# Kernel tuning notes

Hardware: AMD Instinct MI355X
Metric: run time of the kernel (lower is better)

## Reference

```python
import jax, jax.numpy as jnp
import numpy as np

MSG_DIM = 100
REG_WEIGHT = 1.0
N_NODES = 100000
N_EDGES = 1000000
D_FEAT = 6
HIDDEN = 300
OUT_DIM = 2


def setup_inputs() -> dict:
    key = jax.random.key(0)
    ks = jax.random.split(key, 10)
    def glorot(k, shape):
        fan_in = shape[0]
        return jax.random.normal(k, shape, dtype=jnp.float32) / jnp.sqrt(jnp.float32(fan_in))
    return {
        "x": jax.random.normal(ks[0], (N_NODES, D_FEAT), dtype=jnp.float32),
        "edge_index": jax.random.randint(ks[1], (2, N_EDGES), 0, N_NODES, dtype=jnp.int64)
            if jax.config.jax_enable_x64 else jax.random.randint(ks[1], (2, N_EDGES), 0, N_NODES, dtype=jnp.int32),
        "y": jax.random.normal(ks[2], (N_NODES, OUT_DIM), dtype=jnp.float32),
        "target": jax.random.normal(ks[3], (N_NODES, OUT_DIM), dtype=jnp.float32),
        "W1": glorot(ks[4], (2 * D_FEAT, HIDDEN)),
        "b1": jnp.zeros((HIDDEN,), dtype=jnp.float32),
        "W2": glorot(ks[5], (HIDDEN, HIDDEN)),
        "b2": jnp.zeros((HIDDEN,), dtype=jnp.float32),
        "W3": glorot(ks[6], (HIDDEN, 2 * MSG_DIM)),
        "b3": jnp.zeros((2 * MSG_DIM,), dtype=jnp.float32),
    }


def reference(x, edge_index, y, target, W1, b1, W2, b2, W3, b3):
    # MAE term: sum |y - target| / n_nodes
    base_loss = jnp.sum(jnp.abs(y - target)) / y.shape[0]
    # Gather sender/receiver node features per edge and concat -> [E, 2*d_feat]
    e = jnp.concatenate([x[edge_index[0]], x[edge_index[1]]], axis=1)
    # edge_model MLP: 2*d_feat -> 300 -> 300 -> 2*msg_dim
    h = jax.nn.relu(e @ W1 + b1)
    h = jax.nn.relu(h @ W2 + b2)
    messages = h @ W3 + b3  # [E, 2*msg_dim]
    mu = messages[:, :MSG_DIM]
    logvar = messages[:, MSG_DIM:]
    kl_reg = jnp.sum(0.5 * (mu * mu + jnp.exp(logvar) - logvar - 1.0)) / messages.shape[0]
    return base_loss + REG_WEIGHT * kl_reg
```

## Files before the change

kernel.cpp:

```cpp
#include <hip/hip_runtime.h>

#define N_NODES 100000
#define N_EDGES 1000000
#define D_FEAT  6
#define HIDDEN  300
#define HID_P   320
#define MSG     100
#define OUTC    200
#define OUTC_P  208
#define MT      64
#define NT_H    (HID_P/16)
#define NT_M    (OUTC_P/16)
#define KS_H    (HID_P/32)

typedef __bf16 bf16_t;
typedef __bf16 bf16x8 __attribute__((ext_vector_type(8)));
typedef __bf16 bf16x4 __attribute__((ext_vector_type(4)));
typedef float  floatx4 __attribute__((ext_vector_type(4)));

#define PREP_BLOCKS 700
#define LOSS_BLOCKS 200
__global__ void prep_kernel(const float* __restrict__ W1, const float* __restrict__ W2,
                            const float* __restrict__ W3, bf16_t* __restrict__ W1P,
                            bf16_t* __restrict__ W2P, bf16_t* __restrict__ W3P,
                            const float* __restrict__ y, const float* __restrict__ t,
                            float* __restrict__ out) {
    if (blockIdx.x >= PREP_BLOCKS) {
        float s = 0.f;
        for (int i = (blockIdx.x - PREP_BLOCKS) * blockDim.x + threadIdx.x;
             i < N_NODES * 2; i += LOSS_BLOCKS * blockDim.x)
            s += fabsf(y[i] - t[i]);
        #pragma unroll
        for (int off = 32; off; off >>= 1) s += __shfl_down(s, off);
        __shared__ float red[4];
        if ((threadIdx.x & 63) == 0) red[threadIdx.x >> 6] = s;
        __syncthreads();
        if (threadIdx.x == 0)
            atomicAdd(out, (red[0] + red[1] + red[2] + red[3]) * (1.0f / N_NODES));
        return;
    }
    const int n1 = NT_H * 512;
    const int n2 = NT_H * KS_H * 512;
    const int n3 = NT_M * KS_H * 512;
    const int total = n1 + n2 + n3;
    for (int id = blockIdx.x * blockDim.x + threadIdx.x; id < total;
         id += PREP_BLOCKS * blockDim.x) {
        if (id < n1) {
            int nt = id >> 9, rem = id & 511, lane = rem >> 3, j = rem & 7;
            int n = nt * 16 + (lane & 15), k = (lane >> 4) * 8 + j;
            float v = (n < HIDDEN && k < 2 * D_FEAT) ? W1[k * HIDDEN + n] : 0.f;
            W1P[id] = (bf16_t)v;
        } else if (id < n1 + n2) {
            int r = id - n1;
            int chunk = r >> 9, rem = r & 511, lane = rem >> 3, j = rem & 7;
            int ks = chunk % KS_H, nt = chunk / KS_H;
            int n = nt * 16 + (lane & 15), k = ks * 32 + (lane >> 4) * 8 + j;
            float v = (n < HIDDEN && k < HIDDEN) ? W2[k * HIDDEN + n] : 0.f;
            W2P[r] = (bf16_t)v;
        } else {
            int r = id - n1 - n2;
            int chunk = r >> 9, rem = r & 511, lane = rem >> 3, j = rem & 7;
            int ks = chunk % KS_H, nt = chunk / KS_H;
            int n = nt * 16 + (lane & 15), k = ks * 32 + (lane >> 4) * 8 + j;
            float v = (n < OUTC && k < HIDDEN) ? W3[k * OUTC + n] : 0.f;
            W3P[r] = (bf16_t)v;
        }
    }
}

__global__ __launch_bounds__(512, 6) void mlp_kernel(
    const float* __restrict__ x, const int* __restrict__ ei,
    const bf16_t* __restrict__ W1P, const bf16_t* __restrict__ W2P,
    const bf16_t* __restrict__ W3P,
    const float* __restrict__ b1, const float* __restrict__ b2,
    const float* __restrict__ b3, float* __restrict__ out) {
    __shared__ __align__(16) bf16_t A1f[4 * 64 * 8];
    __shared__ __align__(16) bf16_t Hf[4 * KS_H * 64 * 8];
    __shared__ float red[8];

    const int tid  = threadIdx.x;
    const int w    = tid >> 6, lane = tid & 63;
    const int q    = lane >> 4, l16 = lane & 15;
    const int cnt_h = (w < 4) ? 3 : 2;
    const int cnt_m = (w >= 3) ? 2 : 1;
    const long e0 = (long)blockIdx.x * MT;

    *(ulong*)&A1f[tid * 4] = 0ul;
    __syncthreads();
    if (tid < 2 * MT) {
        int m = tid >> 1, side = tid & 1;
        int node = ei[(long)side * N_EDGES + e0 + m];
        const float* xr = x + (long)node * D_FEAT;
        int et = m >> 4, ml = m & 15;
        #pragma unroll
        for (int c = 0; c < D_FEAT; c++) {
            int k = side * D_FEAT + c;
            int lp = ml + 16 * (k >> 3);
            A1f[(et * 64 + lp) * 8 + (k & 7)] = (bf16_t)xr[c];
        }
    }
    __syncthreads();

    floatx4 acc1[3][4];
    {
        bf16x8 hb[4];
        #pragma unroll
        for (int e = 0; e < 4; e++)
            hb[e] = *(const bf16x8*)&A1f[(e * 64 + lane) * 8];
        #pragma unroll
        for (int t = 0; t < 3; t++) {
            if (t < cnt_h) {
                bf16x8 wf = *(const bf16x8*)&W1P[((w + 8 * t) * 64 + lane) * 8];
                #pragma unroll
                for (int e = 0; e < 4; e++) {
                    floatx4 z = {0.f, 0.f, 0.f, 0.f};
                    acc1[t][e] = __builtin_amdgcn_mfma_f32_16x16x32_bf16(wf, hb[e], z, 0, 0, 0);
                }
            }
        }
    }
    #pragma unroll
    for (int t = 0; t < 3; t++) {
        if (t < cnt_h) {
            int n0 = (w + 8 * t) * 16 + 4 * q;
            floatx4 bv = (n0 < HIDDEN) ? *(const floatx4*)&b1[n0]
                                       : (floatx4){0.f, 0.f, 0.f, 0.f};
            int ks = n0 >> 5, lp = l16 + 16 * ((n0 >> 3) & 3), j0 = n0 & 7;
            #pragma unroll
            for (int e = 0; e < 4; e++) {
                bf16x4 pk;
                #pragma unroll
                for (int r = 0; r < 4; r++)
                    pk[r] = (bf16_t)fmaxf(acc1[t][e][r] + bv[r], 0.f);
                *(bf16x4*)&Hf[((e * KS_H + ks) * 64 + lp) * 8 + j0] = pk;
            }
        }
    }
    __syncthreads();

    floatx4 acc2[3][4];
    #pragma unroll
    for (int t = 0; t < 3; t++)
        #pragma unroll
        for (int e = 0; e < 4; e++) acc2[t][e] = (floatx4){0.f, 0.f, 0.f, 0.f};
    #pragma unroll 2
    for (int ks = 0; ks < KS_H; ks++) {
        bf16x8 hb[4];
        #pragma unroll
        for (int e = 0; e < 4; e++)
            hb[e] = *(const bf16x8*)&Hf[((e * KS_H + ks) * 64 + lane) * 8];
        #pragma unroll
        for (int t = 0; t < 3; t++) {
            if (t < cnt_h) {
                bf16x8 wf = *(const bf16x8*)&W2P[(((w + 8 * t) * KS_H + ks) * 64 + lane) * 8];
                #pragma unroll
                for (int e = 0; e < 4; e++)
                    acc2[t][e] = __builtin_amdgcn_mfma_f32_16x16x32_bf16(wf, hb[e], acc2[t][e], 0, 0, 0);
            }
        }
    }
    __syncthreads();
    #pragma unroll
    for (int t = 0; t < 3; t++) {
        if (t < cnt_h) {
            int n0 = (w + 8 * t) * 16 + 4 * q;
            floatx4 bv = (n0 < HIDDEN) ? *(const floatx4*)&b2[n0]
                                       : (floatx4){0.f, 0.f, 0.f, 0.f};
            int ks = n0 >> 5, lp = l16 + 16 * ((n0 >> 3) & 3), j0 = n0 & 7;
            #pragma unroll
            for (int e = 0; e < 4; e++) {
                bf16x4 pk;
                #pragma unroll
                for (int r = 0; r < 4; r++)
                    pk[r] = (bf16_t)fmaxf(acc2[t][e][r] + bv[r], 0.f);
                *(bf16x4*)&Hf[((e * KS_H + ks) * 64 + lp) * 8 + j0] = pk;
            }
        }
    }
    __syncthreads();

    floatx4 acc3[2][4];
    #pragma unroll
    for (int t = 0; t < 2; t++)
        #pragma unroll
        for (int e = 0; e < 4; e++) acc3[t][e] = (floatx4){0.f, 0.f, 0.f, 0.f};
    #pragma unroll 2
    for (int ks = 0; ks < KS_H; ks++) {
        bf16x8 hb[4];
        #pragma unroll
        for (int e = 0; e < 4; e++)
            hb[e] = *(const bf16x8*)&Hf[((e * KS_H + ks) * 64 + lane) * 8];
        #pragma unroll
        for (int t = 0; t < 2; t++) {
            if (t < cnt_m) {
                bf16x8 wf = *(const bf16x8*)&W3P[(((w + 5 * t) * KS_H + ks) * 64 + lane) * 8];
                #pragma unroll
                for (int e = 0; e < 4; e++)
                    acc3[t][e] = __builtin_amdgcn_mfma_f32_16x16x32_bf16(wf, hb[e], acc3[t][e], 0, 0, 0);
            }
        }
    }
    float s = 0.f;
    #pragma unroll
    for (int t = 0; t < 2; t++) {
        if (t < cnt_m) {
            int n0 = (w + 5 * t) * 16 + 4 * q;
            if (n0 < OUTC) {
                floatx4 bv = *(const floatx4*)&b3[n0];
                bool is_mu = (n0 < MSG);
                #pragma unroll
                for (int e = 0; e < 4; e++)
                    #pragma unroll
                    for (int r = 0; r < 4; r++) {
                        float v = acc3[t][e][r] + bv[r];
                        if (is_mu) s += 0.5f * v * v;
                        else       s += 0.5f * (__expf(v) - v - 1.f);
                    }
            }
        }
    }
    #pragma unroll
    for (int off = 32; off; off >>= 1) s += __shfl_down(s, off);
    if (lane == 0) red[w] = s;
    __syncthreads();
    if (tid == 0) {
        float t2 = 0.f;
        #pragma unroll
        for (int i = 0; i < 8; i++) t2 += red[i];
        atomicAdd(out, t2 * (1.0f / N_EDGES));
    }
}

extern "C" void kernel_launch(void* const* d_in, const int* in_sizes, int n_in,
                              void* d_out, int out_size, void* d_ws, size_t ws_size,
                              hipStream_t stream) {
    const float* x      = (const float*)d_in[0];
    const int*   ei     = (const int*)d_in[1];
    const float* y      = (const float*)d_in[2];
    const float* target = (const float*)d_in[3];
    const float* W1     = (const float*)d_in[4];
    const float* b1     = (const float*)d_in[5];
    const float* W2     = (const float*)d_in[6];
    const float* b2     = (const float*)d_in[7];
    const float* W3     = (const float*)d_in[8];
    const float* b3     = (const float*)d_in[9];
    float* out = (float*)d_out;

    bf16_t* W1P = (bf16_t*)d_ws;
    bf16_t* W2P = W1P + NT_H * 512;
    bf16_t* W3P = W2P + NT_H * KS_H * 512;

    hipMemsetAsync(d_out, 0, sizeof(float), stream);
    prep_kernel<<<PREP_BLOCKS + LOSS_BLOCKS, 256, 0, stream>>>(
        W1, W2, W3, W1P, W2P, W3P, y, target, out);
    mlp_kernel<<<N_EDGES / MT, 512, 0, stream>>>(x, ei, W1P, W2P, W3P, b1, b2, b3, out);
}
```

Before: 458.8 us.

## Halve MLP block to four waves with balanced column tiles and aliased LDS

The MLP kernel now runs 256 threads (4 waves) per block instead of 512. Each wave handles 5 hidden column tiles, uniformly and without per-wave counts, and up to 4 output tiles, so the earlier 3/2 and 2/1 imbalance between waves goes away. The input staging buffer and the reduction scratch now alias the hidden LDS buffer, and the ks loops are no longer unrolled by two. The aim is better wave balance and more resident blocks per CU through less LDS. The cost is more accumulators per wave (5x4 floatx4 per layer), which raises register pressure and may lower occupancy.

After: 888.6 us. 93.7% more time.

```diff
diff --git a/kernel.cpp b/kernel.cpp
--- a/kernel.cpp
+++ b/kernel.cpp
@@ -7,10 +7,9 @@
 #define HID_P   320
 #define MSG     100
 #define OUTC    200
-#define OUTC_P  208
 #define MT      64
 #define NT_H    (HID_P/16)
-#define NT_M    (OUTC_P/16)
+#define NT_M    13
 #define KS_H    (HID_P/32)
 
 typedef __bf16 bf16_t;
@@ -68,24 +67,21 @@
     }
 }
 
-__global__ __launch_bounds__(512, 6) void mlp_kernel(
+__global__ __launch_bounds__(256, 4) void mlp_kernel(
     const float* __restrict__ x, const int* __restrict__ ei,
     const bf16_t* __restrict__ W1P, const bf16_t* __restrict__ W2P,
     const bf16_t* __restrict__ W3P,
     const float* __restrict__ b1, const float* __restrict__ b2,
     const float* __restrict__ b3, float* __restrict__ out) {
-    __shared__ __align__(16) bf16_t A1f[4 * 64 * 8];
     __shared__ __align__(16) bf16_t Hf[4 * KS_H * 64 * 8];
-    __shared__ float red[8];
+    bf16_t* A1f = Hf;
 
     const int tid  = threadIdx.x;
     const int w    = tid >> 6, lane = tid & 63;
     const int q    = lane >> 4, l16 = lane & 15;
-    const int cnt_h = (w < 4) ? 3 : 2;
-    const int cnt_m = (w >= 3) ? 2 : 1;
     const long e0 = (long)blockIdx.x * MT;
 
-    *(ulong*)&A1f[tid * 4] = 0ul;
+    ((uint4*)A1f)[tid] = (uint4){0u, 0u, 0u, 0u};
     __syncthreads();
     if (tid < 2 * MT) {
         int m = tid >> 1, side = tid & 1;
@@ -101,99 +97,90 @@
     }
     __syncthreads();
 
-    floatx4 acc1[3][4];
+    floatx4 acc1[5][4];
     {
         bf16x8 hb[4];
         #pragma unroll
         for (int e = 0; e < 4; e++)
             hb[e] = *(const bf16x8*)&A1f[(e * 64 + lane) * 8];
         #pragma unroll
-        for (int t = 0; t < 3; t++) {
-            if (t < cnt_h) {
-                bf16x8 wf = *(const bf16x8*)&W1P[((w + 8 * t) * 64 + lane) * 8];
-                #pragma unroll
-                for (int e = 0; e < 4; e++) {
-                    floatx4 z = {0.f, 0.f, 0.f, 0.f};
-                    acc1[t][e] = __builtin_amdgcn_mfma_f32_16x16x32_bf16(wf, hb[e], z, 0, 0, 0);
-                }
+        for (int t = 0; t < 5; t++) {
+            bf16x8 wf = *(const bf16x8*)&W1P[((w + 4 * t) * 64 + lane) * 8];
+            #pragma unroll
+            for (int e = 0; e < 4; e++) {
+                floatx4 z = {0.f, 0.f, 0.f, 0.f};
+                acc1[t][e] = __builtin_amdgcn_mfma_f32_16x16x32_bf16(wf, hb[e], z, 0, 0, 0);
             }
         }
-    }
-    #pragma unroll
-    for (int t = 0; t < 3; t++) {
-        if (t < cnt_h) {
-            int n0 = (w + 8 * t) * 16 + 4 * q;
-            floatx4 bv = (n0 < HIDDEN) ? *(const floatx4*)&b1[n0]
-                                       : (floatx4){0.f, 0.f, 0.f, 0.f};
-            int ks = n0 >> 5, lp = l16 + 16 * ((n0 >> 3) & 3), j0 = n0 & 7;
-            #pragma unroll
-            for (int e = 0; e < 4; e++) {
-                bf16x4 pk;
-                #pragma unroll
-                for (int r = 0; r < 4; r++)
-                    pk[r] = (bf16_t)fmaxf(acc1[t][e][r] + bv[r], 0.f);
-                *(bf16x4*)&Hf[((e * KS_H + ks) * 64 + lp) * 8 + j0] = pk;
-            }
-        }
-    }
-    __syncthreads();
-
-    floatx4 acc2[3][4];
-    #pragma unroll
-    for (int t = 0; t < 3; t++)
+        __syncthreads();
+    }
+    #pragma unroll
+    for (int t = 0; t < 5; t++) {
+        int n0 = (w + 4 * t) * 16 + 4 * q;
+        floatx4 bv = (n0 < HIDDEN) ? *(const floatx4*)&b1[n0]
+                                   : (floatx4){0.f, 0.f, 0.f, 0.f};
+        int ks = n0 >> 5, lp = l16 + 16 * ((n0 >> 3) & 3), j0 = n0 & 7;
+        #pragma unroll
+        for (int e = 0; e < 4; e++) {
+            bf16x4 pk;
+            #pragma unroll
+            for (int r = 0; r < 4; r++)
+                pk[r] = (bf16_t)fmaxf(acc1[t][e][r] + bv[r], 0.f);
+            *(bf16x4*)&Hf[((e * KS_H + ks) * 64 + lp) * 8 + j0] = pk;
+        }
+    }
+    __syncthreads();
+
+    floatx4 acc2[5][4];
+    #pragma unroll
+    for (int t = 0; t < 5; t++)
         #pragma unroll
         for (int e = 0; e < 4; e++) acc2[t][e] = (floatx4){0.f, 0.f, 0.f, 0.f};
-    #pragma unroll 2
     for (int ks = 0; ks < KS_H; ks++) {
         bf16x8 hb[4];
         #pragma unroll
         for (int e = 0; e < 4; e++)
             hb[e] = *(const bf16x8*)&Hf[((e * KS_H + ks) * 64 + lane) * 8];
         #pragma unroll
-        for (int t = 0; t < 3; t++) {
-            if (t < cnt_h) {
-                bf16x8 wf = *(const bf16x8*)&W2P[(((w + 8 * t) * KS_H + ks) * 64 + lane) * 8];
-                #pragma unroll
-                for (int e = 0; e < 4; e++)
-                    acc2[t][e] = __builtin_amdgcn_mfma_f32_16x16x32_bf16(wf, hb[e], acc2[t][e], 0, 0, 0);
-            }
-        }
-    }
-    __syncthreads();
-    #pragma unroll
-    for (int t = 0; t < 3; t++) {
-        if (t < cnt_h) {
-            int n0 = (w + 8 * t) * 16 + 4 * q;
-            floatx4 bv = (n0 < HIDDEN) ? *(const floatx4*)&b2[n0]
-                                       : (floatx4){0.f, 0.f, 0.f, 0.f};
-            int ks = n0 >> 5, lp = l16 + 16 * ((n0 >> 3) & 3), j0 = n0 & 7;
-            #pragma unroll
-            for (int e = 0; e < 4; e++) {
-                bf16x4 pk;
-                #pragma unroll
-                for (int r = 0; r < 4; r++)
-                    pk[r] = (bf16_t)fmaxf(acc2[t][e][r] + bv[r], 0.f);
-                *(bf16x4*)&Hf[((e * KS_H + ks) * 64 + lp) * 8 + j0] = pk;
-            }
-        }
-    }
-    __syncthreads();
-
-    floatx4 acc3[2][4];
-    #pragma unroll
-    for (int t = 0; t < 2; t++)
+        for (int t = 0; t < 5; t++) {
+            bf16x8 wf = *(const bf16x8*)&W2P[(((w + 4 * t) * KS_H + ks) * 64 + lane) * 8];
+            #pragma unroll
+            for (int e = 0; e < 4; e++)
+                acc2[t][e] = __builtin_amdgcn_mfma_f32_16x16x32_bf16(wf, hb[e], acc2[t][e], 0, 0, 0);
+        }
+    }
+    __syncthreads();
+    #pragma unroll
+    for (int t = 0; t < 5; t++) {
+        int n0 = (w + 4 * t) * 16 + 4 * q;
+        floatx4 bv = (n0 < HIDDEN) ? *(const floatx4*)&b2[n0]
+                                   : (floatx4){0.f, 0.f, 0.f, 0.f};
+        int ks = n0 >> 5, lp = l16 + 16 * ((n0 >> 3) & 3), j0 = n0 & 7;
+        #pragma unroll
+        for (int e = 0; e < 4; e++) {
+            bf16x4 pk;
+            #pragma unroll
+            for (int r = 0; r < 4; r++)
+                pk[r] = (bf16_t)fmaxf(acc2[t][e][r] + bv[r], 0.f);
+            *(bf16x4*)&Hf[((e * KS_H + ks) * 64 + lp) * 8 + j0] = pk;
+        }
+    }
+    __syncthreads();
+
+    floatx4 acc3[4][4];
+    #pragma unroll
+    for (int t = 0; t < 4; t++)
         #pragma unroll
         for (int e = 0; e < 4; e++) acc3[t][e] = (floatx4){0.f, 0.f, 0.f, 0.f};
-    #pragma unroll 2
     for (int ks = 0; ks < KS_H; ks++) {
         bf16x8 hb[4];
         #pragma unroll
         for (int e = 0; e < 4; e++)
             hb[e] = *(const bf16x8*)&Hf[((e * KS_H + ks) * 64 + lane) * 8];
         #pragma unroll
-        for (int t = 0; t < 2; t++) {
-            if (t < cnt_m) {
-                bf16x8 wf = *(const bf16x8*)&W3P[(((w + 5 * t) * KS_H + ks) * 64 + lane) * 8];
+        for (int t = 0; t < 4; t++) {
+            if (w + 4 * t < NT_M) {
+                bf16x8 wf = *(const bf16x8*)&W3P[(((w + 4 * t) * KS_H + ks) * 64 + lane) * 8];
                 #pragma unroll
                 for (int e = 0; e < 4; e++)
                     acc3[t][e] = __builtin_amdgcn_mfma_f32_16x16x32_bf16(wf, hb[e], acc3[t][e], 0, 0, 0);
@@ -202,9 +189,9 @@
     }
     float s = 0.f;
     #pragma unroll
-    for (int t = 0; t < 2; t++) {
-        if (t < cnt_m) {
-            int n0 = (w + 5 * t) * 16 + 4 * q;
+    for (int t = 0; t < 4; t++) {
+        if (w + 4 * t < NT_M) {
+            int n0 = (w + 4 * t) * 16 + 4 * q;
             if (n0 < OUTC) {
                 floatx4 bv = *(const floatx4*)&b3[n0];
                 bool is_mu = (n0 < MSG);
@@ -221,14 +208,12 @@
     }
     #pragma unroll
     for (int off = 32; off; off >>= 1) s += __shfl_down(s, off);
+    __syncthreads();
+    float* red = (float*)Hf;
     if (lane == 0) red[w] = s;
     __syncthreads();
-    if (tid == 0) {
-        float t2 = 0.f;
-        #pragma unroll
-        for (int i = 0; i < 8; i++) t2 += red[i];
-        atomicAdd(out, t2 * (1.0f / N_EDGES));
-    }
+    if (tid == 0)
+        atomicAdd(out, (red[0] + red[1] + red[2] + red[3]) * (1.0f / N_EDGES));
 }
 
 extern "C" void kernel_launch(void* const* d_in, const int* in_sizes, int n_in,
@@ -253,5 +238,5 @@
     hipMemsetAsync(d_out, 0, sizeof(float), stream);
     prep_kernel<<<PREP_BLOCKS + LOSS_BLOCKS, 256, 0, stream>>>(
         W1, W2, W3, W1P, W2P, W3P, y, target, out);
-    mlp_kernel<<<N_EDGES / MT, 512, 0, stream>>>(x, ei, W1P, W2P, W3P, b1, b2, b3, out);
+    mlp_kernel<<<N_EDGES / MT, 256, 0, stream>>>(x, ei, W1P, W2P, W3P, b1, b2, b3, out);
 }
```
